# Kernel optimization log

Measured on AMD Instinct MI355X. Metric: run time of the kernel, lower is better.

The kernel has to match this reference:

```python
import jax, jax.numpy as jnp
import numpy as np

W = 131072          # window size (number of observed frames)
J = 21              # number of joints
B = J - 1           # number of bones
F, PX, PY = 512.0, 512.0, 288.0   # pinhole intrinsics (SIZE_X=1024, SIZE_Y=576)
EPS = 1e-8
WEIGHTS = {"proj": 0.25, "lift": 0.25, "bone": 0.25, "smooth": 0.25}


def _euler_batch(roll, pitch, yaw):
    """Vectorized ZYX euler -> rotation matrices, numpy, [N,3,3]."""
    cr, sr = np.cos(roll), np.sin(roll)
    cp, sp = np.cos(pitch), np.sin(pitch)
    cy, sy = np.cos(yaw), np.sin(yaw)
    R = np.empty(roll.shape + (3, 3), np.float32)
    R[..., 0, 0] = cy * cp; R[..., 0, 1] = cy * sp * sr - sy * cr; R[..., 0, 2] = cy * sp * cr + sy * sr
    R[..., 1, 0] = sy * cp; R[..., 1, 1] = sy * sp * sr + cy * cr; R[..., 1, 2] = sy * sp * cr - cy * sr
    R[..., 2, 0] = -sp;     R[..., 2, 1] = cp * sr;                R[..., 2, 2] = cp * cr
    return R


def setup_inputs() -> dict:
    key = jax.random.key(0)
    ks = jax.random.split(key, 7)
    pose3d = jax.random.normal(ks[0], (W + 1, 3, J), jnp.float32)
    bone_2d = jax.random.normal(ks[1], (W, 2, J), jnp.float32)
    lift_dirs = jax.random.normal(ks[2], (W, 3, B), jnp.float32)
    # small proper drone rotations so the projection depth stays well away from 0
    ang = 0.05 * np.asarray(jax.random.normal(ks[3], (W, 3)))
    R_drone = jnp.asarray(_euler_batch(ang[:, 0], ang[:, 1], ang[:, 2]))
    # drone positions offset so pose - C_drone ~ +10 in every coordinate
    C_drone = 0.1 * jax.random.normal(ks[4], (W, 3, 1), jnp.float32) - 10.0
    bone_lengths = jax.random.uniform(ks[5], (B,), jnp.float32, 0.5, 1.5)
    R_cam = jnp.asarray(_euler_batch(np.zeros(1), np.full(1, np.pi / 2), np.zeros(1))[0])
    # chain skeleton: bone i connects joint i+1 -> joint i
    bone_connections = jnp.stack([jnp.arange(1, J, dtype=jnp.int32),
                                  jnp.arange(0, J - 1, dtype=jnp.int32)], axis=1)
    return {"pose3d": pose3d, "bone_2d": bone_2d, "lift_dirs": lift_dirs,
            "R_drone": R_drone, "C_drone": C_drone, "bone_lengths": bone_lengths,
            "R_cam": R_cam, "bone_connections": bone_connections}


def _forward(pose3d, bone_2d, lift_dirs, R_drone, C_drone, bone_lengths, R_cam,
             bone_connections):
    Jn = pose3d.shape[2]
    b0 = bone_connections[:, 0]
    b1 = bone_connections[:, 1]
    p = pose3d[1:]                                   # [W,3,J] frames with observations

    # ---- projection loss: cam = R_cam @ R_drone^T @ (p - C_drone), pinhole
    rel = p - C_drone                                # [W,3,J]
    cam = jnp.einsum('ij,wkj,wkn->win', R_cam, R_drone, rel)  # [W,3,J]
    z = cam[:, 2]
    proj2d = jnp.stack([F * cam[:, 0] / z + PX,
                        F * cam[:, 1] / z + PY], axis=1)       # [W,2,J]
    proj_loss = jnp.sum((proj2d - bone_2d) ** 2) / (2 * Jn)

    # ---- lift loss: unit bone direction vectors vs lifted directions
    bv = p[:, :, b0] - p[:, :, b1]                   # [W,3,B]
    dirs = bv / (jnp.linalg.norm(bv, axis=1, keepdims=True) + EPS)
    lift_loss = jnp.sum((lift_dirs - dirs) ** 2) / (3 * Jn)

    # ---- bone-length loss over all W+1 frames (squared lengths, as in torch code)
    bvall = pose3d[:, :, b0] - pose3d[:, :, b1]      # [W+1,3,B]
    blen = jnp.sum(bvall ** 2, axis=1)               # [W+1,B]
    bone_loss = jnp.sum((bone_lengths[None, :] - blen) ** 2) / (Jn - 1)

    # ---- smoothness: second difference of the pose trajectory
    d = pose3d[1:] - pose3d[:-1]                     # [W,3,J]
    smooth_loss = jnp.sum((d[1:] - d[:-1]) ** 2) / (3 * Jn)

    return (WEIGHTS["proj"] * proj_loss + WEIGHTS["lift"] * lift_loss
            + WEIGHTS["bone"] * bone_loss + WEIGHTS["smooth"] * smooth_loss)


def reference(pose3d, bone_2d, lift_dirs, R_drone, C_drone, bone_lengths, R_cam,
              bone_connections):
    return _forward(pose3d, bone_2d, lift_dirs, R_drone, C_drone, bone_lengths,
                    R_cam, bone_connections)
```

## Files before the change

### kernel.cpp

```cpp
#include <hip/hip_runtime.h>

namespace {

constexpr int JN = 21;
constexpr int BN = 20;
constexpr int FR = 64;

constexpr float F_F  = 512.0f;
constexpr float PX_F = 512.0f;
constexpr float PY_F = 288.0f;
constexpr float EPS_F = 1e-8f;

constexpr float WPROJ   = 0.25f / (2.0f * 21.0f);
constexpr float WLIFT   = 0.25f / (3.0f * 21.0f);
constexpr float WBONE   = 0.25f / 20.0f;
constexpr float WSMOOTH = 0.25f / (3.0f * 21.0f);

__device__ __forceinline__ double block_reduce(double val) {
    __shared__ double smem[16];
    const int lane = threadIdx.x & 63;
    const int wid  = threadIdx.x >> 6;
    #pragma unroll
    for (int off = 32; off > 0; off >>= 1)
        val += __shfl_down(val, off, 64);
    if (lane == 0) smem[wid] = val;
    __syncthreads();
    if (wid == 0) {
        const int nw = blockDim.x >> 6;
        val = (lane < nw) ? smem[lane] : 0.0;
        #pragma unroll
        for (int off = 32; off > 0; off >>= 1)
            val += __shfl_down(val, off, 64);
    }
    return val;
}

__global__ __launch_bounds__(256) void pose_loss_kernel(
    const float* __restrict__ pose3d,
    const float* __restrict__ bone_2d,
    const float* __restrict__ lift_dirs,
    const float* __restrict__ R_drone,
    const float* __restrict__ C_drone,
    const float* __restrict__ bone_len,
    const float* __restrict__ R_cam,
    float* __restrict__ partials,
    int W)
{
    __shared__ alignas(16) float s_pose[(FR + 2) * 63 + 2];
    __shared__ alignas(16) float s_M[FR * 9];
    __shared__ alignas(16) float s_MC[FR * 3];

    const int tid = threadIdx.x;
    const int w0  = blockIdx.x * FR;
    const int nF  = min(FR, W - w0);
    const int nPoseF = min(FR + 2, W + 1 - w0);

    {
        const float* src = pose3d + (size_t)w0 * 63;
        const int nfl = nPoseF * 63;
        const int n4 = nfl >> 2;
        const float4* s4 = (const float4*)src;
        float4* d4 = (float4*)s_pose;
        for (int i = tid; i < n4; i += 256) d4[i] = s4[i];
        for (int i = (n4 << 2) + tid; i < nfl; i += 256) s_pose[i] = src[i];
    }
    {
        const float* src = R_drone + (size_t)w0 * 9;
        const int nfl = nF * 9;
        const int n4 = nfl >> 2;
        const float4* s4 = (const float4*)src;
        float4* d4 = (float4*)s_M;
        for (int i = tid; i < n4; i += 256) d4[i] = s4[i];
        for (int i = (n4 << 2) + tid; i < nfl; i += 256) s_M[i] = src[i];
    }
    {
        const float* src = C_drone + (size_t)w0 * 3;
        const int nfl = nF * 3;
        const int n4 = nfl >> 2;
        const float4* s4 = (const float4*)src;
        float4* d4 = (float4*)s_MC;
        for (int i = tid; i < n4; i += 256) d4[i] = s4[i];
        for (int i = (n4 << 2) + tid; i < nfl; i += 256) s_MC[i] = src[i];
    }
    __syncthreads();

    if (tid < nF) {
        float Rd[9];
        #pragma unroll
        for (int k = 0; k < 9; ++k) Rd[k] = s_M[tid * 9 + k];
        float rc[9];
        #pragma unroll
        for (int k = 0; k < 9; ++k) rc[k] = R_cam[k];
        float M[9];
        #pragma unroll
        for (int i = 0; i < 3; ++i)
            #pragma unroll
            for (int k = 0; k < 3; ++k)
                M[i * 3 + k] = rc[i * 3 + 0] * Rd[k * 3 + 0]
                             + rc[i * 3 + 1] * Rd[k * 3 + 1]
                             + rc[i * 3 + 2] * Rd[k * 3 + 2];
        const float C0 = s_MC[tid * 3 + 0];
        const float C1 = s_MC[tid * 3 + 1];
        const float C2 = s_MC[tid * 3 + 2];
        #pragma unroll
        for (int k = 0; k < 9; ++k) s_M[tid * 9 + k] = M[k];
        #pragma unroll
        for (int i = 0; i < 3; ++i)
            s_MC[tid * 3 + i] = M[i * 3 + 0] * C0 + M[i * 3 + 1] * C1 + M[i * 3 + 2] * C2;
    }
    __syncthreads();

    float partial = 0.0f;

    auto body = [&](int idx) {
        const int wl = idx / JN;
        const int j  = idx - wl * JN;
        const int w  = w0 + wl;

        const float* P1 = s_pose + (wl + 1) * 63;
        const float p1x = P1[j];
        const float p1y = P1[JN + j];
        const float p1z = P1[2 * JN + j];

        {
            const float* M  = s_M  + wl * 9;
            const float* MC = s_MC + wl * 3;
            const float c0 = M[0] * p1x + M[1] * p1y + M[2] * p1z - MC[0];
            const float c1 = M[3] * p1x + M[4] * p1y + M[5] * p1z - MC[1];
            const float c2 = M[6] * p1x + M[7] * p1y + M[8] * p1z - MC[2];
            const float invz = 1.0f / c2;
            const float u = F_F * c0 * invz + PX_F;
            const float v = F_F * c1 * invz + PY_F;
            const float du = u - bone_2d[(size_t)w * 42 + j];
            const float dv = v - bone_2d[(size_t)w * 42 + JN + j];
            partial += WPROJ * (du * du + dv * dv);
        }

        if (j < BN) {
            const int b0 = j + 1;
            const int b1 = j;
            {
                const float ax = P1[b0]          - P1[b1];
                const float ay = P1[JN + b0]     - P1[JN + b1];
                const float az = P1[2 * JN + b0] - P1[2 * JN + b1];
                const float inv = 1.0f / (sqrtf(ax * ax + ay * ay + az * az) + EPS_F);
                const float lx = lift_dirs[(size_t)w * 60 + j]           - ax * inv;
                const float ly = lift_dirs[(size_t)w * 60 + BN + j]      - ay * inv;
                const float lz = lift_dirs[(size_t)w * 60 + 2 * BN + j]  - az * inv;
                partial += WLIFT * (lx * lx + ly * ly + lz * lz);
            }
            const float blj = bone_len[j];
            {
                const float* P0 = s_pose + wl * 63;
                const float bx = P0[b0]          - P0[b1];
                const float by = P0[JN + b0]     - P0[JN + b1];
                const float bz = P0[2 * JN + b0] - P0[2 * JN + b1];
                const float bl = bx * bx + by * by + bz * bz;
                const float e = blj - bl;
                partial += WBONE * (e * e);
            }
            if (w == W - 1) {
                const float bx = P1[b0]          - P1[b1];
                const float by = P1[JN + b0]     - P1[JN + b1];
                const float bz = P1[2 * JN + b0] - P1[2 * JN + b1];
                const float bl = bx * bx + by * by + bz * bz;
                const float e = blj - bl;
                partial += WBONE * (e * e);
            }
        }

        if (w < W - 1) {
            const float* P0 = s_pose + wl * 63;
            const float* P2 = s_pose + (wl + 2) * 63;
            const float sx = P2[j]          - 2.0f * p1x + P0[j];
            const float sy = P2[JN + j]     - 2.0f * p1y + P0[JN + j];
            const float sz = P2[2 * JN + j] - 2.0f * p1z + P0[2 * JN + j];
            partial += WSMOOTH * (sx * sx + sy * sy + sz * sz);
        }
    };

    if (nF == FR) {
        #pragma unroll
        for (int k = 0; k < 5; ++k) body(tid + k * 256);
        if (tid < FR * JN - 5 * 256) body(5 * 256 + tid);
    } else {
        for (int idx = tid; idx < nF * JN; idx += 256) body(idx);
    }

    const double bsum = block_reduce((double)partial);
    if (tid == 0) partials[blockIdx.x] = (float)bsum;
}

__global__ __launch_bounds__(256) void final_reduce_kernel(
    const float* __restrict__ partials, float* __restrict__ out, int n)
{
    double v = 0.0;
    for (int i = threadIdx.x; i < n; i += blockDim.x)
        v += (double)partials[i];
    v = block_reduce(v);
    if (threadIdx.x == 0) out[0] = (float)v;
}

}

extern "C" void kernel_launch(void* const* d_in, const int* in_sizes, int n_in,
                              void* d_out, int out_size, void* d_ws, size_t ws_size,
                              hipStream_t stream) {
    const float* pose3d    = (const float*)d_in[0];
    const float* bone_2d   = (const float*)d_in[1];
    const float* lift_dirs = (const float*)d_in[2];
    const float* R_drone   = (const float*)d_in[3];
    const float* C_drone   = (const float*)d_in[4];
    const float* bone_len  = (const float*)d_in[5];
    const float* R_cam     = (const float*)d_in[6];
    float* out = (float*)d_out;
    float* partials = (float*)d_ws;

    const int W = in_sizes[3] / 9;
    const int grid = (W + FR - 1) / FR;

    pose_loss_kernel<<<grid, 256, 0, stream>>>(
        pose3d, bone_2d, lift_dirs, R_drone, C_drone, bone_len, R_cam, partials, W);
    final_reduce_kernel<<<1, 256, 0, stream>>>(partials, out, grid);
}
```

Before: 27.78 us.

## Prefetch per-item inputs into registers and fuse final reduction via last-block counter

Loads the per-item bone_2d and lift_dirs values into registers before the shared-memory staging, so their global latency overlaps with the pose/rotation copies. The separate final-reduce kernel is replaced by an atomic counter, and the last block to finish sums all partials. A memset of the counter is added to the stream, and launch bounds now request 4 blocks per SM. Register pressure goes up from holding 30 prefetched values, and an extra memset launch replaces the second kernel launch.

```diff
diff --git a/kernel.cpp b/kernel.cpp
--- a/kernel.cpp
+++ b/kernel.cpp
@@ -35,7 +35,7 @@
     return val;
 }
 
-__global__ __launch_bounds__(256) void pose_loss_kernel(
+__global__ __launch_bounds__(256, 4) void pose_loss_kernel(
     const float* __restrict__ pose3d,
     const float* __restrict__ bone_2d,
     const float* __restrict__ lift_dirs,
@@ -44,16 +44,40 @@
     const float* __restrict__ bone_len,
     const float* __restrict__ R_cam,
     float* __restrict__ partials,
+    unsigned int* __restrict__ counter,
+    float* __restrict__ out,
     int W)
 {
     __shared__ alignas(16) float s_pose[(FR + 2) * 63 + 2];
     __shared__ alignas(16) float s_M[FR * 9];
     __shared__ alignas(16) float s_MC[FR * 3];
+    __shared__ unsigned int s_isLast;
 
     const int tid = threadIdx.x;
     const int w0  = blockIdx.x * FR;
     const int nF  = min(FR, W - w0);
     const int nPoseF = min(FR + 2, W + 1 - w0);
+    const bool full = (nF == FR);
+
+    float bu[6], bv[6], l0[6], l1[6], l2[6];
+    if (full) {
+        #pragma unroll
+        for (int k = 0; k < 6; ++k) {
+            if (k < 5 || tid < FR * JN - 5 * 256) {
+                const int idx = k * 256 + tid;
+                const int wl = idx / JN;
+                const int j  = idx - wl * JN;
+                const size_t w = (size_t)(w0 + wl);
+                bu[k] = bone_2d[w * 42 + j];
+                bv[k] = bone_2d[w * 42 + JN + j];
+                if (j < BN) {
+                    l0[k] = lift_dirs[w * 60 + j];
+                    l1[k] = lift_dirs[w * 60 + BN + j];
+                    l2[k] = lift_dirs[w * 60 + 2 * BN + j];
+                }
+            }
+        }
+    }
 
     {
         const float* src = pose3d + (size_t)w0 * 63;
@@ -66,21 +90,19 @@
     }
     {
         const float* src = R_drone + (size_t)w0 * 9;
-        const int nfl = nF * 9;
-        const int n4 = nfl >> 2;
+        const int n4 = (nF * 9) >> 2;
         const float4* s4 = (const float4*)src;
         float4* d4 = (float4*)s_M;
         for (int i = tid; i < n4; i += 256) d4[i] = s4[i];
-        for (int i = (n4 << 2) + tid; i < nfl; i += 256) s_M[i] = src[i];
+        for (int i = (n4 << 2) + tid; i < nF * 9; i += 256) s_M[i] = src[i];
     }
     {
         const float* src = C_drone + (size_t)w0 * 3;
-        const int nfl = nF * 3;
-        const int n4 = nfl >> 2;
+        const int n4 = (nF * 3) >> 2;
         const float4* s4 = (const float4*)src;
         float4* d4 = (float4*)s_MC;
         for (int i = tid; i < n4; i += 256) d4[i] = s4[i];
-        for (int i = (n4 << 2) + tid; i < nfl; i += 256) s_MC[i] = src[i];
+        for (int i = (n4 << 2) + tid; i < nF * 3; i += 256) s_MC[i] = src[i];
     }
     __syncthreads();
 
@@ -112,7 +134,7 @@
 
     float partial = 0.0f;
 
-    auto body = [&](int idx) {
+    auto item = [&](int idx, float buk, float bvk, float l0k, float l1k, float l2k) {
         const int wl = idx / JN;
         const int j  = idx - wl * JN;
         const int w  = w0 + wl;
@@ -131,8 +153,8 @@
             const float invz = 1.0f / c2;
             const float u = F_F * c0 * invz + PX_F;
             const float v = F_F * c1 * invz + PY_F;
-            const float du = u - bone_2d[(size_t)w * 42 + j];
-            const float dv = v - bone_2d[(size_t)w * 42 + JN + j];
+            const float du = u - buk;
+            const float dv = v - bvk;
             partial += WPROJ * (du * du + dv * dv);
         }
 
@@ -144,9 +166,9 @@
                 const float ay = P1[JN + b0]     - P1[JN + b1];
                 const float az = P1[2 * JN + b0] - P1[2 * JN + b1];
                 const float inv = 1.0f / (sqrtf(ax * ax + ay * ay + az * az) + EPS_F);
-                const float lx = lift_dirs[(size_t)w * 60 + j]           - ax * inv;
-                const float ly = lift_dirs[(size_t)w * 60 + BN + j]      - ay * inv;
-                const float lz = lift_dirs[(size_t)w * 60 + 2 * BN + j]  - az * inv;
+                const float lx = l0k - ax * inv;
+                const float ly = l1k - ay * inv;
+                const float lz = l2k - az * inv;
                 partial += WLIFT * (lx * lx + ly * ly + lz * lz);
             }
             const float blj = bone_len[j];
@@ -179,26 +201,47 @@
         }
     };
 
-    if (nF == FR) {
-        #pragma unroll
-        for (int k = 0; k < 5; ++k) body(tid + k * 256);
-        if (tid < FR * JN - 5 * 256) body(5 * 256 + tid);
+    if (full) {
+        #pragma unroll
+        for (int k = 0; k < 6; ++k) {
+            if (k < 5 || tid < FR * JN - 5 * 256)
+                item(k * 256 + tid, bu[k], bv[k], l0[k], l1[k], l2[k]);
+        }
     } else {
-        for (int idx = tid; idx < nF * JN; idx += 256) body(idx);
+        for (int idx = tid; idx < nF * JN; idx += 256) {
+            const int wl = idx / JN;
+            const int j  = idx - wl * JN;
+            const size_t w = (size_t)(w0 + wl);
+            const float xbu = bone_2d[w * 42 + j];
+            const float xbv = bone_2d[w * 42 + JN + j];
+            float xl0 = 0.f, xl1 = 0.f, xl2 = 0.f;
+            if (j < BN) {
+                xl0 = lift_dirs[w * 60 + j];
+                xl1 = lift_dirs[w * 60 + BN + j];
+                xl2 = lift_dirs[w * 60 + 2 * BN + j];
+            }
+            item(idx, xbu, xbv, xl0, xl1, xl2);
+        }
     }
 
     const double bsum = block_reduce((double)partial);
-    if (tid == 0) partials[blockIdx.x] = (float)bsum;
-}
-
-__global__ __launch_bounds__(256) void final_reduce_kernel(
-    const float* __restrict__ partials, float* __restrict__ out, int n)
-{
-    double v = 0.0;
-    for (int i = threadIdx.x; i < n; i += blockDim.x)
-        v += (double)partials[i];
-    v = block_reduce(v);
-    if (threadIdx.x == 0) out[0] = (float)v;
+
+    if (tid == 0) {
+        __hip_atomic_store(&partials[blockIdx.x], (float)bsum,
+                           __ATOMIC_RELEASE, __HIP_MEMORY_SCOPE_AGENT);
+        const unsigned int c = __hip_atomic_fetch_add(counter, 1u,
+                           __ATOMIC_ACQ_REL, __HIP_MEMORY_SCOPE_AGENT);
+        s_isLast = (c == gridDim.x - 1) ? 1u : 0u;
+    }
+    __syncthreads();
+    if (s_isLast) {
+        double v = 0.0;
+        for (int i = tid; i < (int)gridDim.x; i += 256)
+            v += (double)__hip_atomic_load(&partials[i],
+                           __ATOMIC_ACQUIRE, __HIP_MEMORY_SCOPE_AGENT);
+        v = block_reduce(v);
+        if (tid == 0) out[0] = (float)v;
+    }
 }
 
 }
@@ -214,12 +257,16 @@
     const float* bone_len  = (const float*)d_in[5];
     const float* R_cam     = (const float*)d_in[6];
     float* out = (float*)d_out;
-    float* partials = (float*)d_ws;
 
     const int W = in_sizes[3] / 9;
     const int grid = (W + FR - 1) / FR;
 
+    float* partials = (float*)d_ws;
+    unsigned int* counter = (unsigned int*)((char*)d_ws + ((size_t)grid * 4 + 255) / 256 * 256);
+
+    hipMemsetAsync(counter, 0, sizeof(unsigned int), stream);
+
     pose_loss_kernel<<<grid, 256, 0, stream>>>(
-        pose3d, bone_2d, lift_dirs, R_drone, C_drone, bone_len, R_cam, partials, W);
-    final_reduce_kernel<<<1, 256, 0, stream>>>(partials, out, grid);
-}
+        pose3d, bone_2d, lift_dirs, R_drone, C_drone, bone_len, R_cam,
+        partials, counter, out, W);
+}
```

Result: slower. 100.00 us (+259.9%).

## Split block tile into two halves to overlap staging with compute

Applied to the files above, without the earlier changes.

Splits each block's 64-frame tile into two halves. The first half's pose frames are staged and its camera matrices computed, and after one barrier the second half's loads are issued while the first half's loss items are computed. Camera matrices are now built directly from global R_drone/C_drone instead of being staged in shared memory first, which removes one barrier. This aims to overlap global load latency with arithmetic, at the cost of an extra barrier between halves and less fully unrolled item loops.

```diff
diff --git a/kernel.cpp b/kernel.cpp
--- a/kernel.cpp
+++ b/kernel.cpp
@@ -5,6 +5,8 @@
 constexpr int JN = 21;
 constexpr int BN = 20;
 constexpr int FR = 64;
+constexpr int HT = 32;
+constexpr int SPLIT0 = 36;
 
 constexpr float F_F  = 512.0f;
 constexpr float PX_F = 512.0f;
@@ -55,67 +57,46 @@
     const int nF  = min(FR, W - w0);
     const int nPoseF = min(FR + 2, W + 1 - w0);
 
-    {
-        const float* src = pose3d + (size_t)w0 * 63;
-        const int nfl = nPoseF * 63;
+    auto stage4 = [&](float* dst, const float* src, int nfl) {
         const int n4 = nfl >> 2;
         const float4* s4 = (const float4*)src;
-        float4* d4 = (float4*)s_pose;
+        float4* d4 = (float4*)dst;
         for (int i = tid; i < n4; i += 256) d4[i] = s4[i];
-        for (int i = (n4 << 2) + tid; i < nfl; i += 256) s_pose[i] = src[i];
-    }
-    {
-        const float* src = R_drone + (size_t)w0 * 9;
-        const int nfl = nF * 9;
-        const int n4 = nfl >> 2;
-        const float4* s4 = (const float4*)src;
-        float4* d4 = (float4*)s_M;
-        for (int i = tid; i < n4; i += 256) d4[i] = s4[i];
-        for (int i = (n4 << 2) + tid; i < nfl; i += 256) s_M[i] = src[i];
-    }
-    {
-        const float* src = C_drone + (size_t)w0 * 3;
-        const int nfl = nF * 3;
-        const int n4 = nfl >> 2;
-        const float4* s4 = (const float4*)src;
-        float4* d4 = (float4*)s_MC;
-        for (int i = tid; i < n4; i += 256) d4[i] = s4[i];
-        for (int i = (n4 << 2) + tid; i < nfl; i += 256) s_MC[i] = src[i];
-    }
-    __syncthreads();
-
-    if (tid < nF) {
-        float Rd[9];
-        #pragma unroll
-        for (int k = 0; k < 9; ++k) Rd[k] = s_M[tid * 9 + k];
-        float rc[9];
-        #pragma unroll
-        for (int k = 0; k < 9; ++k) rc[k] = R_cam[k];
-        float M[9];
-        #pragma unroll
-        for (int i = 0; i < 3; ++i)
-            #pragma unroll
-            for (int k = 0; k < 3; ++k)
-                M[i * 3 + k] = rc[i * 3 + 0] * Rd[k * 3 + 0]
-                             + rc[i * 3 + 1] * Rd[k * 3 + 1]
-                             + rc[i * 3 + 2] * Rd[k * 3 + 2];
-        const float C0 = s_MC[tid * 3 + 0];
-        const float C1 = s_MC[tid * 3 + 1];
-        const float C2 = s_MC[tid * 3 + 2];
-        #pragma unroll
-        for (int k = 0; k < 9; ++k) s_M[tid * 9 + k] = M[k];
-        #pragma unroll
-        for (int i = 0; i < 3; ++i)
-            s_MC[tid * 3 + i] = M[i * 3 + 0] * C0 + M[i * 3 + 1] * C1 + M[i * 3 + 2] * C2;
-    }
-    __syncthreads();
+        for (int i = (n4 << 2) + tid; i < nfl; i += 256) dst[i] = src[i];
+    };
+
+    auto computeM = [&](int base) {
+        const int f = base + tid;
+        if (tid < HT && f < nF) {
+            const float* Rd = R_drone + (size_t)(w0 + f) * 9;
+            float rd[9];
+            #pragma unroll
+            for (int k = 0; k < 9; ++k) rd[k] = Rd[k];
+            float rc[9];
+            #pragma unroll
+            for (int k = 0; k < 9; ++k) rc[k] = R_cam[k];
+            float M[9];
+            #pragma unroll
+            for (int i = 0; i < 3; ++i)
+                #pragma unroll
+                for (int k = 0; k < 3; ++k)
+                    M[i * 3 + k] = rc[i * 3 + 0] * rd[k * 3 + 0]
+                                 + rc[i * 3 + 1] * rd[k * 3 + 1]
+                                 + rc[i * 3 + 2] * rd[k * 3 + 2];
+            const float* Cp = C_drone + (size_t)(w0 + f) * 3;
+            const float C0 = Cp[0], C1 = Cp[1], C2 = Cp[2];
+            #pragma unroll
+            for (int k = 0; k < 9; ++k) s_M[f * 9 + k] = M[k];
+            #pragma unroll
+            for (int i = 0; i < 3; ++i)
+                s_MC[f * 3 + i] = M[i * 3 + 0] * C0 + M[i * 3 + 1] * C1 + M[i * 3 + 2] * C2;
+        }
+    };
 
     float partial = 0.0f;
 
-    auto body = [&](int idx) {
-        const int wl = idx / JN;
-        const int j  = idx - wl * JN;
-        const int w  = w0 + wl;
+    auto item = [&](int wl, int j) {
+        const int w = w0 + wl;
 
         const float* P1 = s_pose + (wl + 1) * 63;
         const float p1x = P1[j];
@@ -144,9 +125,9 @@
                 const float ay = P1[JN + b0]     - P1[JN + b1];
                 const float az = P1[2 * JN + b0] - P1[2 * JN + b1];
                 const float inv = 1.0f / (sqrtf(ax * ax + ay * ay + az * az) + EPS_F);
-                const float lx = lift_dirs[(size_t)w * 60 + j]           - ax * inv;
-                const float ly = lift_dirs[(size_t)w * 60 + BN + j]      - ay * inv;
-                const float lz = lift_dirs[(size_t)w * 60 + 2 * BN + j]  - az * inv;
+                const float lx = lift_dirs[(size_t)w * 60 + j]          - ax * inv;
+                const float ly = lift_dirs[(size_t)w * 60 + BN + j]     - ay * inv;
+                const float lz = lift_dirs[(size_t)w * 60 + 2 * BN + j] - az * inv;
                 partial += WLIFT * (lx * lx + ly * ly + lz * lz);
             }
             const float blj = bone_len[j];
@@ -179,12 +160,36 @@
         }
     };
 
-    if (nF == FR) {
-        #pragma unroll
-        for (int k = 0; k < 5; ++k) body(tid + k * 256);
-        if (tid < FR * JN - 5 * 256) body(5 * 256 + tid);
-    } else {
-        for (int idx = tid; idx < nF * JN; idx += 256) body(idx);
+    {
+        const int f1 = min(SPLIT0, nPoseF);
+        stage4(s_pose, pose3d + (size_t)w0 * 63, f1 * 63);
+        computeM(0);
+    }
+    __syncthreads();
+
+    if (nPoseF > SPLIT0) {
+        stage4(s_pose + SPLIT0 * 63, pose3d + ((size_t)w0 + SPLIT0) * 63,
+               (nPoseF - SPLIT0) * 63);
+    }
+    computeM(HT);
+
+    {
+        const int nItems0 = min(HT, nF) * JN;
+        for (int it = tid; it < nItems0; it += 256) {
+            const int wl = it / JN;
+            const int j  = it - wl * JN;
+            item(wl, j);
+        }
+    }
+    __syncthreads();
+
+    if (nF > HT) {
+        const int nItems1 = (nF - HT) * JN;
+        for (int it = tid; it < nItems1; it += 256) {
+            const int wl = HT + it / JN;
+            const int j  = it - (it / JN) * JN;
+            item(wl, j);
+        }
     }
 
     const double bsum = block_reduce((double)partial);
```

New measurement: 27.16 us. -2.3%, faster.
